# Kernel tuning notes

Hardware: AMD Instinct MI355X
Metric: run time of the kernel (lower is better)

## Reference

```python
import jax, jax.numpy as jnp
import numpy as np

B, V, K = 4, 16384, 16
E, F, D, H, L, ITERS = 32, 2, 64, 4, 2, 10
NEG = -1e9


def setup_inputs() -> dict:
    key = jax.random.key(0)
    ks = jax.random.split(key, 24)
    def g(k, shape, fan_in):
        return jax.random.normal(k, shape, dtype=jnp.float32) * (fan_in ** -0.5)
    inp = {}
    inp["node_embeddings"] = jax.random.normal(ks[0], (B, V, E), dtype=jnp.float32)
    inp["node_features"] = jax.random.normal(ks[1], (B, V, F), dtype=jnp.float32)
    inp["demands"] = jax.random.normal(ks[2], (B, V, 1), dtype=jnp.float32)
    # padded adjacency list; value == V means masked (no neighbor)
    inp["adj_lst"] = jax.random.randint(ks[3], (B, V, K), 0, V + 1, dtype=jnp.int32)
    # precomputed inverse-adjacency indices; reference computes inflow by scatter-add instead
    inp["flow_indices"] = jax.random.randint(ks[4], (B, V, K), 0, V, dtype=jnp.int32)
    inp["num_nodes"] = V
    din = E + F
    inp["W_enc1"] = g(ks[5], (din, D), din); inp["b_enc1"] = jnp.zeros((D,), jnp.float32)
    inp["W_enc2"] = g(ks[6], (D, D), D); inp["b_enc2"] = jnp.zeros((D,), jnp.float32)
    inp["W_gat"] = g(ks[7], (H, D, D), D)
    inp["a_src"] = g(ks[8], (H, D), D)
    inp["a_dst"] = g(ks[9], (H, D), D)
    for i, nm in enumerate(["z", "r", "c"]):
        inp["W_" + nm] = g(ks[10 + 2 * i], (D, D), D)
        inp["U_" + nm] = g(ks[11 + 2 * i], (D, D), D)
        inp["b_" + nm] = jnp.zeros((D,), jnp.float32)
    inp["W_dec1"] = g(ks[16], (D, D), D); inp["b_dec1"] = jnp.zeros((D,), jnp.float32)
    inp["W_dec2"] = g(ks[17], (D, 1), D); inp["b_dec2"] = jnp.zeros((1,), jnp.float32)
    return inp


def _forward(node_embeddings, node_features, demands,
             W_enc1, b_enc1, W_enc2, b_enc2,
             W_gat, a_src, a_dst,
             W_z, U_z, b_z, W_r, U_r, b_r, W_c, U_c, b_c,
             W_dec1, b_dec1, W_dec2, b_dec2,
             adj_lst, num_nodes):
    Vn = num_nodes
    bidx = jnp.arange(adj_lst.shape[0])[:, None, None]  # [B,1,1]
    mask = adj_lst == Vn  # [B,V,K] padded slots

    # --- node encoder MLP (tanh, activate_final=True) ---
    x = jnp.concatenate([node_embeddings, node_features], axis=-1)
    h = jnp.tanh(x @ W_enc1 + b_enc1)
    h = jnp.tanh(h @ W_enc2 + b_enc2)

    def gather_nodes(t):
        # masked_gather: pad with a zero row so index == num_nodes reads zeros
        t_pad = jnp.concatenate([t, jnp.zeros_like(t[:, :1])], axis=1)  # [B,V+1,Dt]
        return t_pad[bidx, adj_lst]  # [B,V,K,Dt]

    # --- graph_layers x (AdjGAT + GRU) ---
    for _ in range(L):
        agg = 0.0
        for hd in range(H):
            t = h @ W_gat[hd]                       # [B,V,D]
            nb = gather_nodes(t)                    # [B,V,K,D]
            scores = (t @ a_src[hd])[:, :, None] + nb @ a_dst[hd]  # [B,V,K]
            attn = jax.nn.softmax(jnp.where(mask, NEG, scores), axis=-1)
            agg = agg + jnp.einsum('bvk,bvkd->bvd', attn, nb)
        m = jnp.tanh(agg / H)
        z = jax.nn.sigmoid(m @ W_z + h @ U_z + b_z)
        r = jax.nn.sigmoid(m @ W_r + h @ U_r + b_r)
        c = jnp.tanh(m @ W_c + (r * h) @ U_c + b_c)
        h = (1.0 - z) * h + z * c

    # --- decoder -> per-edge weights via masked gather + softmax ---
    node_w = jnp.tanh(h @ W_dec1 + b_dec1) @ W_dec2 + b_dec2   # [B,V,1]
    pw = gather_nodes(node_w)[..., 0]                          # [B,V,K]
    norm_w = jax.nn.softmax(jnp.where(mask, NEG, pw), axis=-1)

    # --- iterative min-cost-flow solver ---
    flow0 = norm_w * jax.nn.relu(-demands)  # sources (demand<0) push supply
    def body(carry, _):
        flow, _ = carry
        inflow = jnp.zeros((flow.shape[0], Vn + 1), flow.dtype)
        inflow = inflow.at[bidx, adj_lst].add(flow)[:, :Vn]    # [B,V]
        new = norm_w * jax.nn.relu(inflow[..., None] - demands)
        return (new, flow), None
    (flow, pflow), _ = jax.lax.scan(body, (flow0, flow0), None, length=ITERS)

    flow_cost = jnp.sum(flow * flow, axis=(1, 2))  # quadratic cost_fn
    return flow, flow_cost, norm_w, pflow


def reference(node_embeddings, node_features, demands, adj_lst, flow_indices, num_nodes,
              W_enc1, b_enc1, W_enc2, b_enc2, W_gat, a_src, a_dst,
              W_z, U_z, b_z, W_r, U_r, b_r, W_c, U_c, b_c,
              W_dec1, b_dec1, W_dec2, b_dec2):
    # flow_indices is the precomputed inverse adjacency; inflow is computed
    # equivalently here by scatter-add over adj_lst.
    return _forward(node_embeddings, node_features, demands,
                    W_enc1, b_enc1, W_enc2, b_enc2,
                    W_gat, a_src, a_dst,
                    W_z, U_z, b_z, W_r, U_r, b_r, W_c, U_c, b_c,
                    W_dec1, b_dec1, W_dec2, b_dec2,
                    adj_lst, num_nodes)
```

## Files before the change

kernel.cpp:

```cpp
#include <hip/hip_runtime.h>
#include <stdint.h>
#include <math.h>

#define BN 4
#define VN 16384
#define KN 16
#define HN 4
#define NN (BN*VN)
#define EN (VN*KN)
#define CAP 64
#define NEGC (-1.0e9f)

typedef __attribute__((ext_vector_type(8))) short short8;
typedef __attribute__((ext_vector_type(4))) float floatx4;
typedef __attribute__((ext_vector_type(2))) float floatx2;
typedef unsigned short u16;
typedef unsigned int u32;

#define OFF_H      0ull
#define OFF_M      8388608ull
#define OFF_T      16777216ull
#define OFF_SS     50331648ull
#define OFF_NW     52428800ull
#define OFF_NV     52690944ull
#define OFF_CNT    53215232ull
#define OFF_PG     53477376ull
#define OFF_PZR    (OFF_PG  + 32768ull)
#define OFF_PC     (OFF_PZR + 32768ull)
#define OFF_PE1    (OFF_PC  + 16384ull)
#define OFF_PE2    (OFF_PE1 + 8192ull)
#define OFF_PD1    (OFF_PE2 + 8192ull)
#define OFF_PAV    (OFF_PD1 + 8192ull)

__device__ __forceinline__ u16 f2bf(float x){
  union { float f; unsigned int u; } c; c.f = x;
  unsigned int r = c.u + 0x7fffu + ((c.u >> 16) & 1u);
  return (u16)(r >> 16);
}
__device__ __forceinline__ float bf2f(u32 s){
  union { unsigned int u; float f; } c; c.u = s << 16;
  return c.f;
}
__device__ __forceinline__ float sigm(float x){ return 1.0f/(1.0f+expf(-x)); }

union S8 { short8 v; u16 u[8]; };

__global__ __launch_bounds__(256) void k_pack(
    const float* __restrict__ Wg,  const float* __restrict__ Wz, const float* __restrict__ Uz,
    const float* __restrict__ Wr,  const float* __restrict__ Ur, const float* __restrict__ Wc,
    const float* __restrict__ Uc,  const float* __restrict__ We1, const float* __restrict__ We2,
    const float* __restrict__ Wd1, const float* __restrict__ asrc, const float* __restrict__ adst,
    u16* __restrict__ pg, u16* __restrict__ pzr, u16* __restrict__ pc,
    u16* __restrict__ pe1, u16* __restrict__ pe2, u16* __restrict__ pd1,
    u16* __restrict__ pav)
{
  int e = blockIdx.x*256 + threadIdx.x;
  if (e >= 54272) return;
  int el; u16* dst; int CN; int region;
  if      (e < 16384){ el = e;        dst = pg;  CN = 2; region = 0; }
  else if (e < 32768){ el = e-16384;  dst = pzr; CN = 4; region = 1; }
  else if (e < 40960){ el = e-32768;  dst = pc;  CN = 4; region = 2; }
  else if (e < 45056){ el = e-40960;  dst = pe1; CN = 2; region = 3; }
  else if (e < 49152){ el = e-45056;  dst = pe2; CN = 2; region = 4; }
  else if (e < 53248){ el = e-49152;  dst = pd1; CN = 2; region = 5; }
  else               { el = e-53248;  dst = pav; CN = 2; region = 6; }
  int j    = el & 7;
  int lane = (el >> 3) & 63;
  int rest = el >> 9;
  int c  = rest % CN;
  int ng = rest / CN;
  int k  = c*32 + (lane>>4)*8 + j;
  int n  = ng*16 + (lane&15);
  float val = 0.0f;
  if (region == 0){
    val = Wg[(size_t)(n>>6)*4096 + k*64 + (n&63)];
  } else if (region == 1){
    int km = (k&3)*16 + ((k>>2)&15);
    if (n < 64) val = (k<64) ? Wz[km*64+n]      : Uz[(k-64)*64+n];
    else        val = (k<64) ? Wr[km*64+(n-64)] : Ur[(k-64)*64+(n-64)];
  } else if (region == 2){
    int km = (k&3)*16 + ((k>>2)&15);
    val = (k<64) ? Wc[km*64+n] : Uc[(k-64)*64+n];
  } else if (region == 3){
    val = (k<34) ? We1[k*64+n] : 0.0f;
  } else if (region == 4){
    val = We2[k*64+n];
  } else if (region == 5){
    val = Wd1[k*64+n];
  } else {
    int hd = (n>>1)&3, s = n&1;
    const float* av = s ? (adst + hd*64) : (asrc + hd*64);
    const float* wrow = Wg + (size_t)hd*4096 + k*64;
    float acc = 0.f;
    #pragma unroll 8
    for (int d=0; d<64; d++) acc += wrow[d]*av[d];
    val = acc;
  }
  dst[el] = f2bf(val);
}

template<int CN>
__device__ __forceinline__ void load_b(const u16* p, int chunk, int lane, short8 Bf[CN][4]){
  const short8* P = (const short8*)p;
  #pragma unroll
  for (int c=0;c<CN;c++)
    #pragma unroll
    for (int ng=0; ng<4; ng++)
      Bf[c][ng] = P[((chunk*4+ng)*CN + c)*64 + lane];
}

template<int CN>
__device__ __forceinline__ void mfma_tile(const short8* A, const short8 Bf[CN][4],
                                          floatx4 acc[4][4], int wave, int lane){
  #pragma unroll
  for (int c=0;c<CN;c++){
    #pragma unroll
    for (int mg=0;mg<4;mg++){
      short8 a = A[((wave*4+mg)*CN + c)*64 + lane];
      #pragma unroll
      for (int ng=0;ng<4;ng++)
        acc[mg][ng] = __builtin_amdgcn_mfma_f32_16x16x32_bf16(a, Bf[c][ng], acc[mg][ng], 0, 0, 0);
    }
  }
}

__device__ __forceinline__ void zero_acc(floatx4 acc[4][4]){
  #pragma unroll
  for (int mg=0;mg<4;mg++)
    #pragma unroll
    for (int ng=0;ng<4;ng++){
      floatx4 z = {0.f,0.f,0.f,0.f};
      acc[mg][ng] = z;
    }
}

__global__ __launch_bounds__(128) void k_enc(
    const float* __restrict__ emb, const float* __restrict__ feat,
    const u16* __restrict__ pe1, const u16* __restrict__ pe2,
    const float* __restrict__ be1, const float* __restrict__ be2,
    u16* __restrict__ hout, u32* __restrict__ cnt)
{
  cnt[blockIdx.x*128 + threadIdx.x] = 0u;
  __shared__ short8 A1[1024];
  __shared__ short8 A2[1024];
  const int tid = threadIdx.x;
  const int n0  = blockIdx.x * 128;
  for (int it=0; it<8; ++it){
    int slot = it*128 + tid;
    int row = slot >> 3, jc = slot & 7;
    S8 w;
    if (jc < 4){
      const float* s = emb + (size_t)(n0+row)*32 + jc*8;
      #pragma unroll
      for (int j=0;j<8;j++) w.u[j] = f2bf(s[j]);
    } else if (jc == 4){
      const float* s = feat + (size_t)(n0+row)*2;
      w.u[0] = f2bf(s[0]); w.u[1] = f2bf(s[1]);
      #pragma unroll
      for (int j=2;j<8;j++) w.u[j] = 0;
    } else {
      #pragma unroll
      for (int j=0;j<8;j++) w.u[j] = 0;
    }
    A1[((row>>4)*2 + (jc>>2))*64 + (jc&3)*16 + (row&15)] = w.v;
  }
  __syncthreads();
  const int wave = tid>>6, lane = tid&63, q = lane>>4, ml = lane&15;

  short8 Bf[2][4];
  load_b<2>(pe1, 0, lane, Bf);
  floatx4 acc[4][4];
  zero_acc(acc);
  mfma_tile<2>(A1, Bf, acc, wave, lane);

  u16* A2s = (u16*)A2;
  #pragma unroll
  for (int mg=0;mg<4;mg++){
    #pragma unroll
    for (int r=0;r<4;r++){
      int row_l = wave*64 + mg*16 + q*4 + r;
      #pragma unroll
      for (int ng=0;ng<4;ng++){
        int k2 = ng*16 + ml;
        float v = tanhf(acc[mg][ng][r] + be1[k2]);
        int c2 = k2>>5, q2=(k2>>3)&3, j2=k2&7;
        A2s[ (((row_l>>4)*2 + c2)*64 + q2*16 + (row_l&15))*8 + j2 ] = f2bf(v);
      }
    }
  }
  __syncthreads();

  load_b<2>(pe2, 0, lane, Bf);
  zero_acc(acc);
  mfma_tile<2>(A2, Bf, acc, wave, lane);
  #pragma unroll
  for (int mg=0;mg<4;mg++)
    #pragma unroll
    for (int r=0;r<4;r++){
      int row = n0 + wave*64 + mg*16 + q*4 + r;
      #pragma unroll
      for (int ng=0;ng<4;ng++){
        int col = ng*16 + ml;
        hout[(size_t)row*64 + col] = f2bf(tanhf(acc[mg][ng][r] + be2[col]));
      }
    }
}

__global__ __launch_bounds__(128) void k_t(
    const u16* __restrict__ h, const u16* __restrict__ pg, const u16* __restrict__ pav,
    u32* __restrict__ tq, float* __restrict__ ss)
{
  __shared__ short8 A[1024];
  const int tid = threadIdx.x;
  const int n0  = blockIdx.x * 128;
  const short8* hp = (const short8*)h;
  for (int it=0; it<8; ++it){
    int slot = it*128 + tid;
    int row = slot >> 3, jc = slot & 7;
    A[((row>>4)*2 + (jc>>2))*64 + (jc&3)*16 + (row&15)] = hp[(size_t)(n0+row)*8 + jc];
  }
  __syncthreads();
  const int wave = tid>>6, lane = tid&63, q = lane>>4, ml = lane&15;

  for (int chunk=0; chunk<4; ++chunk){
    short8 Bf[2][4];
    load_b<2>(pg, chunk, lane, Bf);
    floatx4 acc[4][4];
    zero_acc(acc);
    mfma_tile<2>(A, Bf, acc, wave, lane);

    #pragma unroll
    for (int mg=0;mg<4;mg++){
      #pragma unroll
      for (int r=0;r<4;r++){
        int row = n0 + wave*64 + mg*16 + q*4 + r;
        int pk = __builtin_amdgcn_cvt_pk_fp8_f32(acc[mg][0][r], acc[mg][1][r], 0, false);
        pk     = __builtin_amdgcn_cvt_pk_fp8_f32(acc[mg][2][r], acc[mg][3][r], pk, true);
        tq[(size_t)row*64 + chunk*16 + ml] = (u32)pk;
      }
    }
  }

  const short8* Pv = (const short8*)pav;
  short8 Bs0 = Pv[lane], Bs1 = Pv[64 + lane];
  #pragma unroll
  for (int mg=0;mg<4;mg++){
    floatx4 sacc = {0.f,0.f,0.f,0.f};
    short8 a0 = A[((wave*4+mg)*2 + 0)*64 + lane];
    short8 a1 = A[((wave*4+mg)*2 + 1)*64 + lane];
    sacc = __builtin_amdgcn_mfma_f32_16x16x32_bf16(a0, Bs0, sacc, 0, 0, 0);
    sacc = __builtin_amdgcn_mfma_f32_16x16x32_bf16(a1, Bs1, sacc, 0, 0, 0);
    if (ml < 8){
      #pragma unroll
      for (int r=0;r<4;r++){
        int row = n0 + wave*64 + mg*16 + q*4 + r;
        ss[(size_t)row*8 + ml] = sacc[r];
      }
    }
  }
}

__global__ __launch_bounds__(256) void k_attn(
    const int* __restrict__ adj, const u32* __restrict__ tq,
    const float* __restrict__ ss, u16* __restrict__ m)
{
  const int wave = threadIdx.x>>6, lane = threadIdx.x&63;
  const int bid = blockIdx.x;
  const int b   = (bid & 7) >> 1;
  const int loc = (bid >> 3)*2 + (bid & 1);
  const int nid = b*VN + loc*4 + wave;
  const int hd = lane>>4;
  int u = adj[(size_t)nid*16 + (lane&15)];
  float sc = (u == VN) ? NEGC : (ss[(size_t)nid*8 + hd*2] + ss[((size_t)b*VN + u)*8 + hd*2 + 1]);
  float mx = sc;
  #pragma unroll
  for (int s=1;s<16;s<<=1) mx = fmaxf(mx, __shfl_xor(mx, s, 64));
  float ex = expf(sc - mx);
  float sm = ex;
  #pragma unroll
  for (int s=1;s<16;s<<=1) sm += __shfl_xor(sm, s, 64);
  float attn = ex / sm;

  float a0=0.f, a1=0.f, a2=0.f, a3=0.f;
  const int srcl = lane & 48;
  #pragma unroll
  for (int k2=0;k2<16;k2++){
    int u2 = __shfl(u, k2, 64);
    float av = __shfl(attn, srcl + k2, 64);
    u32 w = tq[((size_t)b*VN + u2)*64 + lane];
    floatx2 f01 = __builtin_amdgcn_cvt_pk_f32_fp8((int)w, false);
    floatx2 f23 = __builtin_amdgcn_cvt_pk_f32_fp8((int)w, true);
    a0 += av*f01.x; a1 += av*f01.y; a2 += av*f23.x; a3 += av*f23.y;
  }
  a0 += __shfl_xor(a0,16,64); a0 += __shfl_xor(a0,32,64);
  a1 += __shfl_xor(a1,16,64); a1 += __shfl_xor(a1,32,64);
  a2 += __shfl_xor(a2,16,64); a2 += __shfl_xor(a2,32,64);
  a3 += __shfl_xor(a3,16,64); a3 += __shfl_xor(a3,32,64);
  if (lane < 16){
    union { uint2 v; u16 u[4]; } val;
    val.u[0] = f2bf(tanhf(a0*0.25f)); val.u[1] = f2bf(tanhf(a1*0.25f));
    val.u[2] = f2bf(tanhf(a2*0.25f)); val.u[3] = f2bf(tanhf(a3*0.25f));
    *(uint2*)(m + (size_t)nid*64 + lane*4) = val.v;
  }
}

__global__ __launch_bounds__(128) void k_gru(
    const u16* __restrict__ m, u16* __restrict__ h,
    const u16* __restrict__ pzr, const u16* __restrict__ pc_,
    const float* __restrict__ bz, const float* __restrict__ br,
    const float* __restrict__ bc_,
    const u16* __restrict__ pd1, const float* __restrict__ bd1,
    const float* __restrict__ Wd2, const float* __restrict__ bd2,
    float* __restrict__ nodew)
{
  __shared__ short8 A[2048];
  const int tid = threadIdx.x;
  const int n0  = blockIdx.x * 128;
  const short8* mp = (const short8*)m;
  const short8* hp = (const short8*)h;
  for (int it=0; it<16; ++it){
    int slot = it*128 + tid;
    int row = slot >> 4, jc = slot & 15;
    short8 w = (jc < 8) ? mp[(size_t)(n0+row)*8 + jc]
                        : hp[(size_t)(n0+row)*8 + (jc-8)];
    A[((row>>4)*4 + (jc>>2))*64 + (jc&3)*16 + (row&15)] = w;
  }
  __syncthreads();
  const int wave = tid>>6, lane = tid&63, q = lane>>4, ml = lane&15;

  short8 Bf[4][4];

  floatx4 zacc[4][4];
  load_b<4>(pzr, 0, lane, Bf);
  zero_acc(zacc);
  mfma_tile<4>(A, Bf, zacc, wave, lane);

  floatx4 acc[4][4];
  load_b<4>(pzr, 1, lane, Bf);
  zero_acc(acc);
  mfma_tile<4>(A, Bf, acc, wave, lane);

  floatx4 h_old[4][4];
  u16* As = (u16*)A;
  #pragma unroll
  for (int mg=0;mg<4;mg++){
    #pragma unroll
    for (int r=0;r<4;r++){
      int row_l = wave*64 + mg*16 + q*4 + r;
      int row   = n0 + row_l;
      #pragma unroll
      for (int ng=0;ng<4;ng++){
        int col = ng*16 + ml;
        float rv = sigm(acc[mg][ng][r] + br[col]);
        float hv = bf2f(h[(size_t)row*64 + col]);
        h_old[mg][ng][r] = hv;
        int kk = 64 + col;
        int c2 = kk>>5, q2 = (kk>>3)&3, j2 = kk&7;
        As[ (((row_l>>4)*4 + c2)*64 + q2*16 + (row_l&15))*8 + j2 ] = f2bf(hv*rv);
      }
    }
  }

  load_b<4>(pc_, 0, lane, Bf);
  zero_acc(acc);
  mfma_tile<4>(A, Bf, acc, wave, lane);

  #pragma unroll
  for (int mg=0;mg<4;mg++)
    #pragma unroll
    for (int r=0;r<4;r++){
      int row_l = wave*64 + mg*16 + q*4 + r;
      int row   = n0 + row_l;
      #pragma unroll
      for (int ng=0;ng<4;ng++){
        int col = ng*16 + ml;
        float zv = sigm(zacc[mg][ng][r] + bz[col]);
        float cv = tanhf(acc[mg][ng][r] + bc_[col]);
        float ho = h_old[mg][ng][r];
        float hn = (1.f - zv)*ho + zv*cv;
        if (nodew == nullptr){
          h[(size_t)row*64 + col] = f2bf(hn);
        } else {
          int kk = 64 + col;
          int c2 = kk>>5, q2 = (kk>>3)&3, j2 = kk&7;
          As[ (((row_l>>4)*4 + c2)*64 + q2*16 + (row_l&15))*8 + j2 ] = f2bf(hn);
        }
      }
    }

  if (nodew){
    short8 Bd[2][4];
    load_b<2>(pd1, 0, lane, Bd);
    floatx4 dacc[4][4];
    zero_acc(dacc);
    #pragma unroll
    for (int c=0;c<2;c++){
      #pragma unroll
      for (int mg=0;mg<4;mg++){
        short8 a = A[((wave*4+mg)*4 + (2+c))*64 + lane];
        #pragma unroll
        for (int ng=0;ng<4;ng++)
          dacc[mg][ng] = __builtin_amdgcn_mfma_f32_16x16x32_bf16(a, Bd[c][ng], dacc[mg][ng], 0, 0, 0);
      }
    }
    float wd2l[4];
    #pragma unroll
    for (int ng=0;ng<4;ng++) wd2l[ng] = Wd2[ng*16 + ml];
    float b2 = bd2[0];
    #pragma unroll
    for (int mg=0;mg<4;mg++)
      #pragma unroll
      for (int r=0;r<4;r++){
        int row = n0 + wave*64 + mg*16 + q*4 + r;
        float ps = 0.f;
        #pragma unroll
        for (int ng=0;ng<4;ng++)
          ps += tanhf(dacc[mg][ng][r] + bd1[ng*16+ml]) * wd2l[ng];
        #pragma unroll
        for (int s=1;s<16;s<<=1) ps += __shfl_xor(ps, s, 64);
        if (ml == 0) nodew[row] = ps + b2;
      }
  }
}

__global__ __launch_bounds__(256) void k_pw(
    const int* __restrict__ adj, const float* __restrict__ nodew, const float* __restrict__ dem,
    float* __restrict__ normw, float* __restrict__ nv0,
    u32* __restrict__ cnt, u32* __restrict__ bucket, float* __restrict__ cost)
{
  if (blockIdx.x == 0 && threadIdx.x < BN) cost[threadIdx.x] = 0.f;
  const int bid = blockIdx.x;
  const int b   = (bid & 7) >> 1;
  const int loc = (bid >> 3)*2 + (bid & 1);
  int node = b*VN + loc*16 + (threadIdx.x >> 4);
  int e = node*16 + (threadIdx.x & 15);
  int u = adj[e];
  float pw = (u == VN) ? NEGC : nodew[(size_t)b*VN + u];
  float mx = pw;
  #pragma unroll
  for (int s=1;s<16;s<<=1) mx = fmaxf(mx, __shfl_xor(mx, s, 64));
  float ex = expf(pw - mx);
  float sm = ex;
  #pragma unroll
  for (int s=1;s<16;s<<=1) sm += __shfl_xor(sm, s, 64);
  float nw = ex / sm;
  normw[e] = nw;
  if ((e & 15) == 0) nv0[node] = fmaxf(-dem[node], 0.f);
  if (u < VN){
    int g = b*VN + u;
    u32 pos = atomicAdd(&cnt[g], 1u);
    if (pos < CAP)
      bucket[(size_t)g*CAP + pos] = ((u32)f2bf(nw) << 16) | (u32)(node & (VN-1));
  }
}

__global__ __launch_bounds__(256) void k_gather(
    const u32* __restrict__ cnt, const u32* __restrict__ bucket,
    const float* __restrict__ dem, const float* __restrict__ nvin, float* __restrict__ nvout,
    const float* __restrict__ normw, float* __restrict__ fout, float* __restrict__ cost)
{
  const int bid = blockIdx.x;
  const int b   = (bid & 7) >> 1;
  const int loc = (bid >> 3)*2 + (bid & 1);
  int g = b*VN + loc*16 + (threadIdx.x >> 4);
  int lane = threadIdx.x & 15;
  u32 n = cnt[g];
  if (n > CAP) n = CAP;
  const u32* bk = bucket + (size_t)g*CAP;
  const float* nb = nvin + (size_t)b*VN;
  float sum = 0.f;
  for (u32 i = (u32)lane; i < n; i += 16u){
    u32 r = bk[i];
    sum += bf2f(r >> 16) * nb[r & 0xFFFFu];
  }
  #pragma unroll
  for (int sh=1; sh<16; sh<<=1) sum += __shfl_xor(sum, sh, 64);
  float nvv = fmaxf(sum - dem[g], 0.f);
  if (lane == 0) nvout[g] = nvv;
  if (fout){
    int e = g*16 + lane;
    float fl = normw[e] * nvv;
    fout[e] = fl;
    if (cost){
      float ssq = fl*fl;
      #pragma unroll
      for (int sh=1; sh<64; sh<<=1) ssq += __shfl_xor(ssq, sh, 64);
      __shared__ float part[4];
      if ((threadIdx.x & 63) == 0) part[threadIdx.x>>6] = ssq;
      __syncthreads();
      if (threadIdx.x == 0) atomicAdd(cost + b, part[0]+part[1]+part[2]+part[3]);
    }
  }
}

extern "C" void kernel_launch(void* const* d_in, const int* in_sizes, int n_in,
                              void* d_out, int out_size, void* d_ws, size_t ws_size,
                              hipStream_t stream)
{
  const float* emb  = (const float*)d_in[0];
  const float* feat = (const float*)d_in[1];
  const float* dem  = (const float*)d_in[2];
  const int*   adj  = (const int*)  d_in[3];
  const float* We1 = (const float*)d_in[6];
  const float* be1 = (const float*)d_in[7];
  const float* We2 = (const float*)d_in[8];
  const float* be2 = (const float*)d_in[9];
  const float* Wg  = (const float*)d_in[10];
  const float* asrc= (const float*)d_in[11];
  const float* adst= (const float*)d_in[12];
  const float* Wz  = (const float*)d_in[13];
  const float* Uz  = (const float*)d_in[14];
  const float* bz  = (const float*)d_in[15];
  const float* Wr  = (const float*)d_in[16];
  const float* Ur  = (const float*)d_in[17];
  const float* br  = (const float*)d_in[18];
  const float* Wc  = (const float*)d_in[19];
  const float* Uc  = (const float*)d_in[20];
  const float* bc  = (const float*)d_in[21];
  const float* Wd1 = (const float*)d_in[22];
  const float* bd1 = (const float*)d_in[23];
  const float* Wd2 = (const float*)d_in[24];
  const float* bd2 = (const float*)d_in[25];

  char* ws = (char*)d_ws;
  u16*   h     = (u16*)  (ws + OFF_H);
  u16*   m     = (u16*)  (ws + OFF_M);
  u32*   tq    = (u32*)  (ws + OFF_T);
  u32*   bucket= (u32*)  (ws + OFF_T);
  float* ss    = (float*)(ws + OFF_SS);
  float* nodew = (float*)(ws + OFF_NW);
  float* nv    = (float*)(ws + OFF_NV);
  u32*   cnt   = (u32*)  (ws + OFF_CNT);
  u16* pg  = (u16*)(ws + OFF_PG);
  u16* pzr = (u16*)(ws + OFF_PZR);
  u16* pc  = (u16*)(ws + OFF_PC);
  u16* pe1 = (u16*)(ws + OFF_PE1);
  u16* pe2 = (u16*)(ws + OFF_PE2);
  u16* pd1 = (u16*)(ws + OFF_PD1);
  u16* pav = (u16*)(ws + OFF_PAV);
  float* nv0b = nv;
  float* nv1b = nv + NN;

  float* out0 = (float*)d_out;
  float* out1 = out0 + 1048576;
  float* out2 = out0 + 1048580;
  float* out3 = out0 + 2097156;

  k_pack<<<212, 256, 0, stream>>>(Wg, Wz, Uz, Wr, Ur, Wc, Uc, We1, We2, Wd1,
                                  asrc, adst, pg, pzr, pc, pe1, pe2, pd1, pav);
  k_enc<<<512, 128, 0, stream>>>(emb, feat, pe1, pe2, be1, be2, h, cnt);

  for (int l=0; l<2; ++l){
    k_t   <<<512, 128, 0, stream>>>(h, pg, pav, tq, ss);
    k_attn<<<16384, 256, 0, stream>>>(adj, tq, ss, m);
    k_gru <<<512, 128, 0, stream>>>(m, h, pzr, pc, bz, br, bc,
                                    pd1, bd1, Wd2, bd2, (l==1) ? nodew : nullptr);
  }

  k_pw <<<4096, 256, 0, stream>>>(adj, nodew, dem, out2, nv0b, cnt, bucket, out1);

  for (int i=1; i<=10; ++i){
    float* in  = (i & 1) ? nv0b : nv1b;
    float* out = (i & 1) ? nv1b : nv0b;
    float* fo  = (i==10) ? out0 : ((i==9) ? out3 : nullptr);
    k_gather<<<4096, 256, 0, stream>>>(cnt, bucket, dem, in, out, out2, fo,
                                       (i==10) ? out1 : nullptr);
  }
}
```

Measured before the change: 444.6 us.

## Fuse flow solver iterations into one cooperative kernel with grid sync

Replaces the softmax/bucket kernel and the ten per-iteration gather kernel launches with a single cooperative kernel of 1024 blocks. Each block handles 64 nodes, and grid.sync() separates the phases and iterations. This removes eleven kernel launch boundaries and their dispatch gaps. In exchange it relies on all blocks being co-resident, and grid-wide barriers have their own cost that can approach a launch gap.

```diff
diff --git a/kernel.cpp b/kernel.cpp
--- a/kernel.cpp
+++ b/kernel.cpp
@@ -1,6 +1,9 @@
 #include <hip/hip_runtime.h>
+#include <hip/hip_cooperative_groups.h>
 #include <stdint.h>
 #include <math.h>
+
+namespace cg = cooperative_groups;
 
 #define BN 4
 #define VN 16384
@@ -423,73 +426,84 @@
   }
 }
 
-__global__ __launch_bounds__(256) void k_pw(
+__global__ __launch_bounds__(256) void k_solver(
     const int* __restrict__ adj, const float* __restrict__ nodew, const float* __restrict__ dem,
-    float* __restrict__ normw, float* __restrict__ nv0,
-    u32* __restrict__ cnt, u32* __restrict__ bucket, float* __restrict__ cost)
-{
-  if (blockIdx.x == 0 && threadIdx.x < BN) cost[threadIdx.x] = 0.f;
+    float* __restrict__ normw, u32* __restrict__ cnt, u32* __restrict__ bucket,
+    float* __restrict__ nv0b, float* __restrict__ nv1b,
+    float* __restrict__ flow, float* __restrict__ pflow, float* __restrict__ cost)
+{
+  cg::grid_group grid = cg::this_grid();
   const int bid = blockIdx.x;
   const int b   = (bid & 7) >> 1;
   const int loc = (bid >> 3)*2 + (bid & 1);
-  int node = b*VN + loc*16 + (threadIdx.x >> 4);
-  int e = node*16 + (threadIdx.x & 15);
-  int u = adj[e];
-  float pw = (u == VN) ? NEGC : nodew[(size_t)b*VN + u];
-  float mx = pw;
-  #pragma unroll
-  for (int s=1;s<16;s<<=1) mx = fmaxf(mx, __shfl_xor(mx, s, 64));
-  float ex = expf(pw - mx);
-  float sm = ex;
-  #pragma unroll
-  for (int s=1;s<16;s<<=1) sm += __shfl_xor(sm, s, 64);
-  float nw = ex / sm;
-  normw[e] = nw;
-  if ((e & 15) == 0) nv0[node] = fmaxf(-dem[node], 0.f);
-  if (u < VN){
-    int g = b*VN + u;
-    u32 pos = atomicAdd(&cnt[g], 1u);
-    if (pos < CAP)
-      bucket[(size_t)g*CAP + pos] = ((u32)f2bf(nw) << 16) | (u32)(node & (VN-1));
-  }
-}
-
-__global__ __launch_bounds__(256) void k_gather(
-    const u32* __restrict__ cnt, const u32* __restrict__ bucket,
-    const float* __restrict__ dem, const float* __restrict__ nvin, float* __restrict__ nvout,
-    const float* __restrict__ normw, float* __restrict__ fout, float* __restrict__ cost)
-{
-  const int bid = blockIdx.x;
-  const int b   = (bid & 7) >> 1;
-  const int loc = (bid >> 3)*2 + (bid & 1);
-  int g = b*VN + loc*16 + (threadIdx.x >> 4);
-  int lane = threadIdx.x & 15;
-  u32 n = cnt[g];
-  if (n > CAP) n = CAP;
-  const u32* bk = bucket + (size_t)g*CAP;
-  const float* nb = nvin + (size_t)b*VN;
-  float sum = 0.f;
-  for (u32 i = (u32)lane; i < n; i += 16u){
-    u32 r = bk[i];
-    sum += bf2f(r >> 16) * nb[r & 0xFFFFu];
-  }
-  #pragma unroll
-  for (int sh=1; sh<16; sh<<=1) sum += __shfl_xor(sum, sh, 64);
-  float nvv = fmaxf(sum - dem[g], 0.f);
-  if (lane == 0) nvout[g] = nvv;
-  if (fout){
-    int e = g*16 + lane;
-    float fl = normw[e] * nvv;
-    fout[e] = fl;
-    if (cost){
-      float ssq = fl*fl;
-      #pragma unroll
-      for (int sh=1; sh<64; sh<<=1) ssq += __shfl_xor(ssq, sh, 64);
+  const int tid = threadIdx.x;
+  const int lane16 = tid & 15;
+  const int g0 = b*VN + loc*64;
+
+  if (bid == 0 && tid < BN) cost[tid] = 0.f;
+
+  #pragma unroll
+  for (int sub=0; sub<4; ++sub){
+    int node = g0 + sub*16 + (tid>>4);
+    int e = node*16 + lane16;
+    int u = adj[e];
+    float pw = (u == VN) ? NEGC : nodew[(size_t)b*VN + u];
+    float mx = pw;
+    #pragma unroll
+    for (int s=1;s<16;s<<=1) mx = fmaxf(mx, __shfl_xor(mx, s, 64));
+    float ex = expf(pw - mx);
+    float sm = ex;
+    #pragma unroll
+    for (int s=1;s<16;s<<=1) sm += __shfl_xor(sm, s, 64);
+    float nw = ex / sm;
+    normw[e] = nw;
+    if (lane16 == 0) nv0b[node] = fmaxf(-dem[node], 0.f);
+    if (u < VN){
+      int g = b*VN + u;
+      u32 pos = atomicAdd(&cnt[g], 1u);
+      if (pos < CAP)
+        bucket[(size_t)g*CAP + pos] = ((u32)f2bf(nw) << 16) | (u32)(node & (VN-1));
+    }
+  }
+  grid.sync();
+
+  for (int it=1; it<=10; ++it){
+    const float* nin = (it & 1) ? nv0b : nv1b;
+    float* nout      = (it & 1) ? nv1b : nv0b;
+    float* fo = (it==10) ? flow : ((it==9) ? pflow : nullptr);
+    float csum = 0.f;
+    #pragma unroll
+    for (int sub=0; sub<4; ++sub){
+      int g = g0 + sub*16 + (tid>>4);
+      u32 n = cnt[g];
+      if (n > CAP) n = CAP;
+      const u32* bk = bucket + (size_t)g*CAP;
+      const float* nb = nin + (size_t)b*VN;
+      float sum = 0.f;
+      for (u32 i = (u32)lane16; i < n; i += 16u){
+        u32 r = bk[i];
+        sum += bf2f(r >> 16) * nb[r & 0xFFFFu];
+      }
+      #pragma unroll
+      for (int sh=1; sh<16; sh<<=1) sum += __shfl_xor(sum, sh, 64);
+      float nvv = fmaxf(sum - dem[g], 0.f);
+      if (lane16 == 0) nout[g] = nvv;
+      if (fo){
+        int e = g*16 + lane16;
+        float fl = normw[e] * nvv;
+        fo[e] = fl;
+        if (it == 10) csum += fl*fl;
+      }
+    }
+    if (it == 10){
+      #pragma unroll
+      for (int sh=1; sh<64; sh<<=1) csum += __shfl_xor(csum, sh, 64);
       __shared__ float part[4];
-      if ((threadIdx.x & 63) == 0) part[threadIdx.x>>6] = ssq;
+      if ((tid & 63) == 0) part[tid>>6] = csum;
       __syncthreads();
-      if (threadIdx.x == 0) atomicAdd(cost + b, part[0]+part[1]+part[2]+part[3]);
-    }
+      if (tid == 0) atomicAdd(cost + b, part[0]+part[1]+part[2]+part[3]);
+    }
+    grid.sync();
   }
 }
 
@@ -557,13 +571,23 @@
                                     pd1, bd1, Wd2, bd2, (l==1) ? nodew : nullptr);
   }
 
-  k_pw <<<4096, 256, 0, stream>>>(adj, nodew, dem, out2, nv0b, cnt, bucket, out1);
-
-  for (int i=1; i<=10; ++i){
-    float* in  = (i & 1) ? nv0b : nv1b;
-    float* out = (i & 1) ? nv1b : nv0b;
-    float* fo  = (i==10) ? out0 : ((i==9) ? out3 : nullptr);
-    k_gather<<<4096, 256, 0, stream>>>(cnt, bucket, dem, in, out, out2, fo,
-                                       (i==10) ? out1 : nullptr);
-  }
-}
+  {
+    const int*   a_adj   = adj;
+    const float* a_nodew = nodew;
+    const float* a_dem   = dem;
+    float* a_normw = out2;
+    u32*   a_cnt   = cnt;
+    u32*   a_bkt   = bucket;
+    float* a_nv0   = nv0b;
+    float* a_nv1   = nv1b;
+    float* a_flow  = out0;
+    float* a_pflow = out3;
+    float* a_cost  = out1;
+    void* kargs[] = { (void*)&a_adj, (void*)&a_nodew, (void*)&a_dem,
+                      (void*)&a_normw, (void*)&a_cnt, (void*)&a_bkt,
+                      (void*)&a_nv0, (void*)&a_nv1,
+                      (void*)&a_flow, (void*)&a_pflow, (void*)&a_cost };
+    hipLaunchCooperativeKernel((void*)k_solver, dim3(1024), dim3(256),
+                               kargs, 0, stream);
+  }
+}
```

After: 1.635 ms. +267.8%, slower.
